# Optimization experiments

Hardware: AMD Instinct MI355X
Metric: run time of the kernel (lower is better)

## Reference

```python
import jax, jax.numpy as jnp
import numpy as np

N_NODES = 20000
NEG_SLOPE = 0.2
EPS = 1e-10


def _gat_reparam_layer(x, W, att_i, att_j, bias, src, dst, heads, c2):
    """GATConv (PyG-style, aggr='add') whose output encodes (mean, std) per head,
    followed by diag-Gaussian reparameterization with N(0,1) prior (eval mode:
    output = mean; ixz = KL(q||p) summed over channels, averaged over heads).
    x: [N, F]; W: [F, heads*c2]; att_i/att_j: [heads, c2]; bias: [heads*c2].
    c2 = 2 * out_channels (mean + std logits).
    Returns out [N, heads*(c2//2)], ixz [N]."""
    N = x.shape[0]
    h = (x @ W).reshape(N, heads, c2)                      # [N, H, 2C]
    h_i = h[dst]                                           # [E, H, 2C] target (x_i)
    h_j = h[src]                                           # [E, H, 2C] source (x_j)
    # attention logits: leaky_relu((x_i*att_i).sum + (x_j*att_j).sum)
    logits = jnp.sum(h_i * att_i, axis=-1) + jnp.sum(h_j * att_j, axis=-1)  # [E, H]
    logits = jax.nn.leaky_relu(logits, NEG_SLOPE)
    # segment softmax over incoming edges of each target node
    lmax = jax.ops.segment_max(logits, dst, num_segments=N)  # [N, H]
    ex = jnp.exp(logits - lmax[dst])                         # [E, H]
    denom = jax.ops.segment_sum(ex, dst, num_segments=N)     # [N, H]
    alpha = ex / denom[dst]                                  # [E, H]
    # weighted scatter-add aggregation
    msg = alpha[:, :, None] * h_j                            # [E, H, 2C]
    out = jax.ops.segment_sum(msg, dst, num_segments=N)      # [N, H, 2C]
    out = out + bias.reshape(1, heads, c2)
    # reparameterization: split per head into mean / std
    C = c2 // 2
    mean = out[..., :C]                                      # [N, H, C]
    std = jax.nn.softplus(out[..., C:]) + EPS                # [N, H, C]
    # KL(N(mean, std) || N(0, 1)) per element, sum over C, mean over heads
    kl = 0.5 * (std * std + mean * mean - 1.0) - jnp.log(std)
    ixz = kl.sum(-1).mean(-1)                                # [N]
    return mean.reshape(N, heads * C), ixz


def setup_inputs() -> dict:
    key = jax.random.key(0)
    ks = jax.random.split(key, 10)
    N, F1 = N_NODES, 256
    E = 320000
    H1, C1 = 8, 32    # conv1: latent_size//2 = 32 per head, doubled for (mean,std)
    H2, C2 = 1, 16    # conv2: num_classes = 16
    edge_index = jax.random.randint(ks[0], (2, E), 0, N, dtype=jnp.int32)
    s = 0.1
    return {
        "x": jax.random.normal(ks[1], (N, F1), jnp.float32),
        "edge_index": edge_index,
        "W1": jax.random.normal(ks[2], (F1, H1 * 2 * C1), jnp.float32) * s,
        "att_i1": jax.random.normal(ks[3], (H1, 2 * C1), jnp.float32) * s,
        "att_j1": jax.random.normal(ks[4], (H1, 2 * C1), jnp.float32) * s,
        "bias1": jax.random.normal(ks[5], (H1 * 2 * C1,), jnp.float32) * s,
        "W2": jax.random.normal(ks[6], (H1 * C1, H2 * 2 * C2), jnp.float32) * s,
        "att_i2": jax.random.normal(ks[7], (H2, 2 * C2), jnp.float32) * s,
        "att_j2": jax.random.normal(ks[8], (H2, 2 * C2), jnp.float32) * s,
        "bias2": jax.random.normal(ks[9], (H2 * 2 * C2,), jnp.float32) * s,
    }


def reference(x, edge_index, W1, att_i1, att_j1, bias1, W2, att_i2, att_j2, bias2):
    src, dst = edge_index[0], edge_index[1]
    # eval mode: dropout is identity, output = posterior mean (val_use_mean=True)
    h1, ixz1 = _gat_reparam_layer(x, W1, att_i1, att_j1, bias1, src, dst, heads=8, c2=64)
    h1 = jax.nn.elu(h1)
    h2, ixz2 = _gat_reparam_layer(h1, W2, att_i2, att_j2, bias2, src, dst, heads=1, c2=32)
    return h2
```

## Files before the change

kernel.cpp:

```cpp
#include <hip/hip_runtime.h>
#include <hip/hip_bf16.h>

#define NN 20000
#define EE 320000
#define NEG_SLOPE 0.2f
#define CAP1 96
#define BCAP 128

typedef unsigned short u16;
typedef short bf16x8 __attribute__((ext_vector_type(8)));
typedef unsigned short u16x8 __attribute__((ext_vector_type(8)));
typedef float f32x4 __attribute__((ext_vector_type(4)));

__device__ __forceinline__ u16 f2bf(float f) {
    unsigned u = __float_as_uint(f);
    return (u16)((u + 0x7FFFu + ((u >> 16) & 1u)) >> 16);
}
__device__ __forceinline__ float bf2f(u16 b) { return __uint_as_float(((unsigned)b) << 16); }

__device__ __forceinline__ void lds_fence() {
    asm volatile("s_waitcnt lgkmcnt(0)" ::: "memory");
}

__device__ __forceinline__ void gld_lds16(const u16* g, u16* l) {
    __builtin_amdgcn_global_load_lds(
        (__attribute__((address_space(1))) void*)g,
        (__attribute__((address_space(3))) void*)l, 16, 0, 0);
}

#define IB_W1 320
#define IB_W2 338
#define IB_CU 417
#define IB_XB 2917
__global__ __launch_bounds__(256) void init_pack(
    const float* __restrict__ x,
    const float* __restrict__ W1, const float* __restrict__ atti1, const float* __restrict__ attj1,
    const float* __restrict__ W2, const float* __restrict__ atti2, const float* __restrict__ attj2,
    u16* __restrict__ Wp1, u16* __restrict__ Wp2, int* __restrict__ cursor, u16* __restrict__ xb)
{
    int b = blockIdx.x;
    if (b < IB_W1) {
        int t = b*256 + threadIdx.x;
        int k = t & 255, j = t >> 8;
        float v = 0.f;
        if (j < 256) {
            v = W1[(size_t)k*512 + ((j>>5)*64 + (j&31))];
        } else if (j < 264) {
            int h = j - 256; float s = 0.f;
            for (int c = 0; c < 64; ++c) s += W1[(size_t)k*512 + h*64 + c] * atti1[h*64 + c];
            v = s;
        } else if (j < 272) {
            int h = j - 264; float s = 0.f;
            for (int c = 0; c < 64; ++c) s += W1[(size_t)k*512 + h*64 + c] * attj1[h*64 + c];
            v = s;
        }
        Wp1[t] = f2bf(v);
    } else if (b < IB_W2) {
        int j = b - IB_W1;
        int k = threadIdx.x;
        float v;
        if (j < 16) {
            v = W2[(size_t)k*32 + j];
        } else if (j == 16) {
            float s = 0.f; for (int c = 0; c < 32; ++c) s += W2[(size_t)k*32 + c] * atti2[c]; v = s;
        } else {
            float s = 0.f; for (int c = 0; c < 32; ++c) s += W2[(size_t)k*32 + c] * attj2[c]; v = s;
        }
        Wp2[j*256 + k] = f2bf(v);
    } else if (b < IB_CU) {
        int i = (b - IB_W2)*256 + threadIdx.x;
        if (i < NN) cursor[i] = 0;
    } else {
        size_t gb = ((size_t)(b - IB_CU)*256 + threadIdx.x) * 8;
        float4 v0 = *(const float4*)&x[gb];
        float4 v1 = *(const float4*)&x[gb + 4];
        u16x8 u;
        u[0]=f2bf(v0.x); u[1]=f2bf(v0.y); u[2]=f2bf(v0.z); u[3]=f2bf(v0.w);
        u[4]=f2bf(v1.x); u[5]=f2bf(v1.y); u[6]=f2bf(v1.z); u[7]=f2bf(v1.w);
        *(u16x8*)&xb[gb] = u;
    }
}

__device__ __forceinline__ void gemm_body(
    int bx, int by, int tid,
    const u16* __restrict__ Ab, const u16* __restrict__ Bp, int M,
    u16* __restrict__ outB, float* __restrict__ outAi, float* __restrict__ outAj)
{
    __shared__ __align__(16) u16 lsA[64*64];
    __shared__ __align__(16) u16 lsB[64*64];

    const int w    = tid >> 6, lane = tid & 63;
    const int brow = by * 64, bcol = bx * 64;

    const int r0 = 2*w*8     + (lane >> 3);
    const int r1 = (2*w+1)*8 + (lane >> 3);
    const int sl = lane & 7;
    const size_t aOff0 = (size_t)min(brow + r0, M-1)*256 + ((sl ^ (r0 & 7))*8);
    const size_t aOff1 = (size_t)min(brow + r1, M-1)*256 + ((sl ^ (r1 & 7))*8);
    const size_t bOff0 = (size_t)(bcol + r0)*256 + ((sl ^ (r0 & 7))*8);
    const size_t bOff1 = (size_t)(bcol + r1)*256 + ((sl ^ (r1 & 7))*8);
    u16* ldsA0 = lsA + (2*w)*512;
    u16* ldsA1 = lsA + (2*w+1)*512;
    u16* ldsB0 = lsB + (2*w)*512;
    u16* ldsB1 = lsB + (2*w+1)*512;

    const int frow = (w << 4) + (lane & 15);
    const int fkb  = lane >> 4;
    int aF[2], bF[2][4];
    #pragma unroll
    for (int v = 0; v < 2; ++v) {
        aF[v] = frow*64 + (((v*4 + fkb) ^ (frow & 7)))*8;
        #pragma unroll
        for (int tt = 0; tt < 4; ++tt) {
            int col = tt*16 + (lane & 15);
            bF[v][tt] = col*64 + (((v*4 + fkb) ^ (col & 7)))*8;
        }
    }

    f32x4 acc[4] = {};

    for (int ks = 0; ks < 4; ++ks) {
        const int k0 = ks*64;
        gld_lds16(Ab + aOff0 + k0, ldsA0);
        gld_lds16(Ab + aOff1 + k0, ldsA1);
        gld_lds16(Bp + bOff0 + k0, ldsB0);
        gld_lds16(Bp + bOff1 + k0, ldsB1);
        __syncthreads();
        #pragma unroll
        for (int v = 0; v < 2; ++v) {
            bf16x8 a = *(const bf16x8*)&lsA[aF[v]];
            #pragma unroll
            for (int tt = 0; tt < 4; ++tt) {
                bf16x8 b = *(const bf16x8*)&lsB[bF[v][tt]];
                acc[tt] = __builtin_amdgcn_mfma_f32_16x16x32_bf16(a, b, acc[tt], 0, 0, 0);
            }
        }
        __syncthreads();
    }

    #pragma unroll
    for (int tt = 0; tt < 4; ++tt) {
        int col = bcol + tt*16 + (lane & 15);
        #pragma unroll
        for (int r = 0; r < 4; ++r) {
            int row = brow + (w << 4) + ((lane >> 4) << 2) + r;
            if (row >= M) continue;
            float v = acc[tt][r];
            if      (col < 256) outB[(size_t)row*256 + col] = f2bf(v);
            else if (col < 264) outAi[(size_t)row*8 + (col - 256)] = v;
            else if (col < 272) outAj[(size_t)row*8 + (col - 264)] = v;
        }
    }
}

#define G1_BLOCKS 1565
#define SC_BLOCKS 1250

__global__ __launch_bounds__(256) void fusedA(
    const u16* __restrict__ xb, const u16* __restrict__ Wp1,
    u16* __restrict__ h1m, float* __restrict__ ai1, float* __restrict__ aj1,
    const int* __restrict__ src, const int* __restrict__ dst,
    int* __restrict__ cursor, int* __restrict__ elist)
{
    int b = blockIdx.x;
    if (b < G1_BLOCKS) {
        gemm_body(b % 5, b / 5, threadIdx.x, xb, Wp1, NN, h1m, ai1, aj1);
    } else {
        int e = (b - G1_BLOCKS)*256 + threadIdx.x;
        if (e < EE) {
            int d = dst[e];
            int pos = atomicAdd(&cursor[d], 1);
            if (pos < BCAP) elist[d*BCAP + pos] = src[e];
        }
    }
}

__global__ __launch_bounds__(256) void gat1g2(
    const int* __restrict__ cursor, const int* __restrict__ elist,
    const float* __restrict__ ai, const float* __restrict__ aj,
    const u16* __restrict__ h1m, const float* __restrict__ bias,
    const u16* __restrict__ Wp2,
    float* __restrict__ h2m, float* __restrict__ ai2, float* __restrict__ aj2)
{
    __shared__ float s_w[4][CAP1*9];
    __shared__ int   s_src[4][CAP1];
    __shared__ float s_inv[4][8];

    const int wv = threadIdx.x >> 6, lane = threadIdx.x & 63;
    const int n = blockIdx.x*4 + wv;
    const int beg = n*BCAP;
    const int deg = min(cursor[n], BCAP);
    float* sw = s_w[wv];
    int*   ss = s_src[wv];

    const int g = lane & 31, head = g >> 2, cbase = (g & 3)*8;
    float v[8];

    if (deg <= CAP1) {
        {
            int hq = lane & 3, eo = lane >> 2;
            float2 aip = *(const float2*)&ai[(size_t)n*8 + hq*2];
            float sm0 = 0.f, sm1 = 0.f;
            for (int e = eo; e < deg; e += 16) {
                int s = elist[beg + e];
                if (hq == 0) ss[e] = s;
                float2 a = *(const float2*)&aj[(size_t)s*8 + hq*2];
                float l0 = aip.x + a.x;
                float l1 = aip.y + a.y;
                l0 = (l0 >= 0.f) ? l0 : NEG_SLOPE * l0;
                l1 = (l1 >= 0.f) ? l1 : NEG_SLOPE * l1;
                float ex0 = __expf(l0), ex1 = __expf(l1);
                sw[e*9 + 2*hq]     = ex0;
                sw[e*9 + 2*hq + 1] = ex1;
                sm0 += ex0; sm1 += ex1;
            }
            #pragma unroll
            for (int o = 4; o <= 32; o <<= 1) {
                sm0 += __shfl_xor(sm0, o, 64);
                sm1 += __shfl_xor(sm1, o, 64);
            }
            if (eo == 0) {
                s_inv[wv][2*hq]     = (deg > 0) ? 1.f / sm0 : 0.f;
                s_inv[wv][2*hq + 1] = (deg > 0) ? 1.f / sm1 : 0.f;
            }
        }
        lds_fence();
        {
            int slot = lane >> 5;
            float inv = s_inv[wv][head];
            const u16* hb = h1m + (size_t)g*8;
            float acc[8] = {};
            int e = slot;
            for (; e + 6 < deg; e += 8) {
                int   i0 = ss[e],          i1 = ss[e+2],          i2 = ss[e+4],          i3 = ss[e+6];
                float w0 = sw[e*9+head],   w1 = sw[(e+2)*9+head], w2 = sw[(e+4)*9+head], w3 = sw[(e+6)*9+head];
                bf16x8 v0 = *(const bf16x8*)&hb[(size_t)i0*256];
                bf16x8 v1 = *(const bf16x8*)&hb[(size_t)i1*256];
                bf16x8 v2 = *(const bf16x8*)&hb[(size_t)i2*256];
                bf16x8 v3 = *(const bf16x8*)&hb[(size_t)i3*256];
                #pragma unroll
                for (int k = 0; k < 8; ++k) {
                    acc[k] += w0 * bf2f((u16)v0[k]);
                    acc[k] += w1 * bf2f((u16)v1[k]);
                    acc[k] += w2 * bf2f((u16)v2[k]);
                    acc[k] += w3 * bf2f((u16)v3[k]);
                }
            }
            for (; e < deg; e += 2) {
                float wgt = sw[e*9 + head];
                bf16x8 vx = *(const bf16x8*)&hb[(size_t)ss[e]*256];
                #pragma unroll
                for (int k = 0; k < 8; ++k)
                    acc[k] += wgt * bf2f((u16)vx[k]);
            }
            #pragma unroll
            for (int k = 0; k < 8; ++k) acc[k] += __shfl_xor(acc[k], 32, 64);
            #pragma unroll
            for (int k = 0; k < 8; ++k) {
                float t = acc[k]*inv + bias[head*64 + cbase + k];
                v[k] = (t > 0.f) ? t : (__expf(t) - 1.0f);
            }
        }
    } else {
        float* sh = sw;
        float4 ai0 = *(const float4*)&ai[(size_t)n*8];
        float4 ai1v = *(const float4*)&ai[(size_t)n*8 + 4];
        float aiv[8] = {ai0.x,ai0.y,ai0.z,ai0.w,ai1v.x,ai1v.y,ai1v.z,ai1v.w};
        for (int h = 0; h < 8; ++h) {
            float a_i = aiv[h];
            float mx = -INFINITY;
            for (int e = lane; e < deg; e += 64) {
                int s = elist[beg + e];
                float t = a_i + aj[(size_t)s*8 + h];
                t = (t >= 0.f) ? t : NEG_SLOPE * t;
                mx = fmaxf(mx, t);
            }
            #pragma unroll
            for (int o = 32; o > 0; o >>= 1) mx = fmaxf(mx, __shfl_xor(mx, o, 64));
            float sm = 0.f;
            for (int e = lane; e < deg; e += 64) {
                int s = elist[beg + e];
                float t = a_i + aj[(size_t)s*8 + h];
                t = (t >= 0.f) ? t : NEG_SLOPE * t;
                sm += __expf(t - mx);
            }
            #pragma unroll
            for (int o = 32; o > 0; o >>= 1) sm += __shfl_xor(sm, o, 64);
            float inv = (deg > 0) ? 1.f / sm : 0.f;
            int c = lane & 31, sl2 = lane >> 5;
            float a2 = 0.f;
            for (int e = sl2; e < deg; e += 2) {
                int s = elist[beg + e];
                float t = a_i + aj[(size_t)s*8 + h];
                t = (t >= 0.f) ? t : NEG_SLOPE * t;
                float wgt = __expf(t - mx);
                a2 += wgt * bf2f(h1m[(size_t)s*256 + h*32 + c]);
            }
            a2 += __shfl_xor(a2, 32, 64);
            if (lane < 32) {
                float t = a2*inv + bias[h*64 + c];
                sh[h*32 + c] = (t > 0.f) ? t : (__expf(t) - 1.0f);
            }
        }
        lds_fence();
        #pragma unroll
        for (int k = 0; k < 8; ++k) v[k] = sh[g*8 + k];
    }

    {
        int jbase = (lane >> 5) * 9;
        float p[9];
        #pragma unroll
        for (int jj = 0; jj < 9; ++jj) {
            u16x8 wr = *(const u16x8*)&Wp2[(size_t)(jbase + jj)*256 + g*8];
            float s = 0.f;
            #pragma unroll
            for (int k = 0; k < 8; ++k) s += v[k] * bf2f((u16)wr[k]);
            p[jj] = s;
        }
        #pragma unroll
        for (int o = 1; o < 32; o <<= 1) {
            #pragma unroll
            for (int jj = 0; jj < 9; ++jj) p[jj] += __shfl_xor(p[jj], o, 64);
        }
        float outv = p[0];
        #pragma unroll
        for (int jj = 1; jj < 9; ++jj) if (g == jj) outv = p[jj];
        if (g < 9) {
            int j = jbase + g;
            if      (j < 16)  h2m[(size_t)n*16 + j] = outv;
            else if (j == 16) ai2[n] = outv;
            else if (j == 17) aj2[n] = outv;
        }
    }
}

__global__ __launch_bounds__(256) void gat2_fused(
    const int* __restrict__ cursor, const int* __restrict__ elist,
    const float* __restrict__ ai, const float* __restrict__ aj,
    const float* __restrict__ h2m, const float* __restrict__ bias,
    float* __restrict__ outp)
{
    __shared__ float s_w2[4][64];
    __shared__ int   s_s2[4][64];

    const int wv = threadIdx.x >> 6, lane = threadIdx.x & 63;
    const int n = blockIdx.x*4 + wv;
    const int beg = n*BCAP;
    const int deg = min(cursor[n], BCAP);
    float a_i = ai[n];

    if (deg <= 64) {
        float ex = 0.f; int s = 0;
        if (lane < deg) {
            s = elist[beg + lane];
            float t = a_i + aj[s];
            t = (t >= 0.f) ? t : NEG_SLOPE * t;
            ex = __expf(t);
        }
        float sm = ex;
        #pragma unroll
        for (int o = 32; o > 0; o >>= 1) sm += __shfl_xor(sm, o, 64);
        float inv = (deg > 0) ? 1.f / sm : 0.f;
        if (lane < deg) { s_w2[wv][lane] = ex; s_s2[wv][lane] = s; }
        lds_fence();
        int c4 = lane & 3, slot = lane >> 2;
        float4 acc = make_float4(0.f, 0.f, 0.f, 0.f);
        for (int e = slot; e < deg; e += 16) {
            float w = s_w2[wv][e];
            int sv = s_s2[wv][e];
            float4 vv = *(const float4*)&h2m[(size_t)sv*16 + c4*4];
            acc.x += w*vv.x; acc.y += w*vv.y; acc.z += w*vv.z; acc.w += w*vv.w;
        }
        #pragma unroll
        for (int o = 4; o <= 32; o <<= 1) {
            acc.x += __shfl_xor(acc.x, o, 64);
            acc.y += __shfl_xor(acc.y, o, 64);
            acc.z += __shfl_xor(acc.z, o, 64);
            acc.w += __shfl_xor(acc.w, o, 64);
        }
        if (lane < 4) {
            const float4 b4 = *(const float4*)&bias[lane*4];
            float4 r = make_float4(acc.x*inv + b4.x, acc.y*inv + b4.y,
                                   acc.z*inv + b4.z, acc.w*inv + b4.w);
            *(float4*)&outp[(size_t)n*16 + lane*4] = r;
        }
    } else {
        float mx = -INFINITY;
        for (int e = lane; e < deg; e += 64) {
            int s2 = elist[beg + e];
            float t = a_i + aj[s2];
            t = (t >= 0.f) ? t : NEG_SLOPE * t;
            mx = fmaxf(mx, t);
        }
        #pragma unroll
        for (int o = 32; o > 0; o >>= 1) mx = fmaxf(mx, __shfl_xor(mx, o, 64));
        float sm = 0.f;
        for (int e = lane; e < deg; e += 64) {
            int s2 = elist[beg + e];
            float t = a_i + aj[s2];
            t = (t >= 0.f) ? t : NEG_SLOPE * t;
            sm += __expf(t - mx);
        }
        #pragma unroll
        for (int o = 32; o > 0; o >>= 1) sm += __shfl_xor(sm, o, 64);
        float inv = (deg > 0) ? 1.f / sm : 0.f;
        int c = lane & 15, e4 = lane >> 4;
        float acc = 0.f;
        for (int e = e4; e < deg; e += 4) {
            int s2 = elist[beg + e];
            float t = a_i + aj[s2];
            t = (t >= 0.f) ? t : NEG_SLOPE * t;
            float w = __expf(t - mx);
            acc += w * h2m[(size_t)s2*16 + c];
        }
        acc += __shfl_xor(acc, 16, 64);
        acc += __shfl_xor(acc, 32, 64);
        if (lane < 16) outp[(size_t)n*16 + lane] = acc*inv + bias[lane];
    }
}

static inline size_t al16(size_t x) { return (x + 15) & ~(size_t)15; }

extern "C" void kernel_launch(void* const* d_in, const int* in_sizes, int n_in,
                              void* d_out, int out_size, void* d_ws, size_t ws_size,
                              hipStream_t stream) {
    const float* x      = (const float*)d_in[0];
    const int*   ei     = (const int*)  d_in[1];
    const float* W1     = (const float*)d_in[2];
    const float* att_i1 = (const float*)d_in[3];
    const float* att_j1 = (const float*)d_in[4];
    const float* bias1  = (const float*)d_in[5];
    const float* W2     = (const float*)d_in[6];
    const float* att_i2 = (const float*)d_in[7];
    const float* att_j2 = (const float*)d_in[8];
    const float* bias2  = (const float*)d_in[9];
    float* out = (float*)d_out;

    const int N = NN, E = EE;
    const int* src = ei;
    const int* dst = ei + E;

    char* p = (char*)d_ws;
    #define CARVE(ty, name, elems) ty* name = (ty*)p; p += al16((size_t)(elems) * sizeof(ty));
    CARVE(u16,   Wp1,  320*256)
    CARVE(u16,   Wp2,  18*256)
    CARVE(u16,   xb,   (size_t)N*256)
    CARVE(u16,   h1m,  (size_t)N*256)
    CARVE(float, ai1,  (size_t)N*8)
    CARVE(float, aj1,  (size_t)N*8)
    CARVE(float, h2m,  (size_t)N*16)
    CARVE(float, ai2,  N)
    CARVE(float, aj2,  N)
    CARVE(int,   cursor,   N)
    CARVE(int,   elist,    (size_t)N*BCAP)
    #undef CARVE

    const int BS = 256;

    init_pack<<<IB_XB, BS, 0, stream>>>(x, W1, att_i1, att_j1, W2, att_i2, att_j2,
                                        Wp1, Wp2, cursor, xb);

    fusedA<<<G1_BLOCKS + SC_BLOCKS, BS, 0, stream>>>(xb, Wp1, h1m, ai1, aj1,
                                                     src, dst, cursor, elist);

    gat1g2<<<N/4, BS, 0, stream>>>(cursor, elist, ai1, aj1, h1m, bias1, Wp2,
                                   h2m, ai2, aj2);

    gat2_fused<<<N/4, BS, 0, stream>>>(cursor, elist, ai2, aj2, h2m, bias2, out);
}
```

Measured before the change: 77.52 us.

## Prefetch neighbor feature gathers before softmax weights in GAT aggregation kernels

Both aggregation kernels now load each edge's source index once per lane and broadcast it with shuffles. The first 16 (layer 1) or all 64 (layer 2) neighbor feature rows are gathered into registers before the attention exponentials and sums are computed, so the gather latency overlaps the softmax work. Layer 1 now computes all 8 heads' logits per lane with a full-wave shuffle reduction in place of the quad-strided LDS layout. CAP1 drops from 96 to 64, which sends nodes with degree 65-96 to the slower general path, and the register prefetch raises VGPR pressure.

```diff
diff --git a/kernel.cpp b/kernel.cpp
--- a/kernel.cpp
+++ b/kernel.cpp
@@ -4,7 +4,7 @@
 #define NN 20000
 #define EE 320000
 #define NEG_SLOPE 0.2f
-#define CAP1 96
+#define CAP1 64
 #define BCAP 128
 
 typedef unsigned short u16;
@@ -184,7 +184,6 @@
 {
     __shared__ float s_w[4][CAP1*9];
     __shared__ int   s_src[4][CAP1];
-    __shared__ float s_inv[4][8];
 
     const int wv = threadIdx.x >> 6, lane = threadIdx.x & 63;
     const int n = blockIdx.x*4 + wv;
@@ -194,72 +193,99 @@
     int*   ss = s_src[wv];
 
     const int g = lane & 31, head = g >> 2, cbase = (g & 3)*8;
+    const int slot = lane >> 5;
     float v[8];
 
     if (deg <= CAP1) {
+        const bool has = lane < deg;
+        int s_own = 0;
+        if (has) s_own = elist[beg + lane];
+        if (has) ss[lane] = s_own;
+
+        float4 a0 = make_float4(0.f,0.f,0.f,0.f), a1 = a0;
+        if (has) {
+            a0 = *(const float4*)&aj[(size_t)s_own*8];
+            a1 = *(const float4*)&aj[(size_t)s_own*8 + 4];
+        }
+
+        const u16* hb = h1m + (size_t)g*8;
+        bf16x8 vv[8];
+        #pragma unroll
+        for (int j = 0; j < 8; ++j) {
+            int ej = slot + 2*j;
+            int sj = __shfl(s_own, ej);
+            if (ej < deg) vv[j] = *(const bf16x8*)&hb[(size_t)sj*256];
+        }
+
+        float4 ai0 = *(const float4*)&ai[(size_t)n*8];
+        float4 ai1v = *(const float4*)&ai[(size_t)n*8 + 4];
+        float ex[8];
         {
-            int hq = lane & 3, eo = lane >> 2;
-            float2 aip = *(const float2*)&ai[(size_t)n*8 + hq*2];
-            float sm0 = 0.f, sm1 = 0.f;
-            for (int e = eo; e < deg; e += 16) {
-                int s = elist[beg + e];
-                if (hq == 0) ss[e] = s;
-                float2 a = *(const float2*)&aj[(size_t)s*8 + hq*2];
-                float l0 = aip.x + a.x;
-                float l1 = aip.y + a.y;
-                l0 = (l0 >= 0.f) ? l0 : NEG_SLOPE * l0;
-                l1 = (l1 >= 0.f) ? l1 : NEG_SLOPE * l1;
-                float ex0 = __expf(l0), ex1 = __expf(l1);
-                sw[e*9 + 2*hq]     = ex0;
-                sw[e*9 + 2*hq + 1] = ex1;
-                sm0 += ex0; sm1 += ex1;
-            }
-            #pragma unroll
-            for (int o = 4; o <= 32; o <<= 1) {
-                sm0 += __shfl_xor(sm0, o, 64);
-                sm1 += __shfl_xor(sm1, o, 64);
-            }
-            if (eo == 0) {
-                s_inv[wv][2*hq]     = (deg > 0) ? 1.f / sm0 : 0.f;
-                s_inv[wv][2*hq + 1] = (deg > 0) ? 1.f / sm1 : 0.f;
-            }
-        }
+            float av[8] = {a0.x,a0.y,a0.z,a0.w,a1.x,a1.y,a1.z,a1.w};
+            float aiv[8] = {ai0.x,ai0.y,ai0.z,ai0.w,ai1v.x,ai1v.y,ai1v.z,ai1v.w};
+            #pragma unroll
+            for (int h = 0; h < 8; ++h) {
+                float l = aiv[h] + av[h];
+                l = (l >= 0.f) ? l : NEG_SLOPE * l;
+                ex[h] = has ? __expf(l) : 0.f;
+                sw[lane*9 + h] = ex[h];
+            }
+        }
+        #pragma unroll
+        for (int o = 1; o <= 32; o <<= 1) {
+            #pragma unroll
+            for (int h = 0; h < 8; ++h) ex[h] += __shfl_xor(ex[h], o, 64);
+        }
+        float smh = ex[0];
+        if (head == 1) smh = ex[1];
+        if (head == 2) smh = ex[2];
+        if (head == 3) smh = ex[3];
+        if (head == 4) smh = ex[4];
+        if (head == 5) smh = ex[5];
+        if (head == 6) smh = ex[6];
+        if (head == 7) smh = ex[7];
+        float inv = (deg > 0) ? 1.f / smh : 0.f;
+
         lds_fence();
-        {
-            int slot = lane >> 5;
-            float inv = s_inv[wv][head];
-            const u16* hb = h1m + (size_t)g*8;
-            float acc[8] = {};
-            int e = slot;
-            for (; e + 6 < deg; e += 8) {
-                int   i0 = ss[e],          i1 = ss[e+2],          i2 = ss[e+4],          i3 = ss[e+6];
-                float w0 = sw[e*9+head],   w1 = sw[(e+2)*9+head], w2 = sw[(e+4)*9+head], w3 = sw[(e+6)*9+head];
-                bf16x8 v0 = *(const bf16x8*)&hb[(size_t)i0*256];
-                bf16x8 v1 = *(const bf16x8*)&hb[(size_t)i1*256];
-                bf16x8 v2 = *(const bf16x8*)&hb[(size_t)i2*256];
-                bf16x8 v3 = *(const bf16x8*)&hb[(size_t)i3*256];
+
+        float acc[8] = {};
+        #pragma unroll
+        for (int j = 0; j < 8; ++j) {
+            int ej = slot + 2*j;
+            if (ej < deg) {
+                float w = sw[ej*9 + head];
                 #pragma unroll
-                for (int k = 0; k < 8; ++k) {
-                    acc[k] += w0 * bf2f((u16)v0[k]);
-                    acc[k] += w1 * bf2f((u16)v1[k]);
-                    acc[k] += w2 * bf2f((u16)v2[k]);
-                    acc[k] += w3 * bf2f((u16)v3[k]);
-                }
-            }
-            for (; e < deg; e += 2) {
-                float wgt = sw[e*9 + head];
-                bf16x8 vx = *(const bf16x8*)&hb[(size_t)ss[e]*256];
-                #pragma unroll
-                for (int k = 0; k < 8; ++k)
-                    acc[k] += wgt * bf2f((u16)vx[k]);
-            }
-            #pragma unroll
-            for (int k = 0; k < 8; ++k) acc[k] += __shfl_xor(acc[k], 32, 64);
+                for (int k = 0; k < 8; ++k) acc[k] += w * bf2f((u16)vv[j][k]);
+            }
+        }
+        int e = 16 + slot;
+        for (; e + 6 < deg; e += 8) {
+            int   i0 = ss[e],          i1 = ss[e+2],          i2 = ss[e+4],          i3 = ss[e+6];
+            float w0 = sw[e*9+head],   w1 = sw[(e+2)*9+head], w2 = sw[(e+4)*9+head], w3 = sw[(e+6)*9+head];
+            bf16x8 v0 = *(const bf16x8*)&hb[(size_t)i0*256];
+            bf16x8 v1 = *(const bf16x8*)&hb[(size_t)i1*256];
+            bf16x8 v2 = *(const bf16x8*)&hb[(size_t)i2*256];
+            bf16x8 v3 = *(const bf16x8*)&hb[(size_t)i3*256];
             #pragma unroll
             for (int k = 0; k < 8; ++k) {
-                float t = acc[k]*inv + bias[head*64 + cbase + k];
-                v[k] = (t > 0.f) ? t : (__expf(t) - 1.0f);
-            }
+                acc[k] += w0 * bf2f((u16)v0[k]);
+                acc[k] += w1 * bf2f((u16)v1[k]);
+                acc[k] += w2 * bf2f((u16)v2[k]);
+                acc[k] += w3 * bf2f((u16)v3[k]);
+            }
+        }
+        for (; e < deg; e += 2) {
+            float wgt = sw[e*9 + head];
+            bf16x8 vx = *(const bf16x8*)&hb[(size_t)ss[e]*256];
+            #pragma unroll
+            for (int k = 0; k < 8; ++k) acc[k] += wgt * bf2f((u16)vx[k]);
+        }
+        #pragma unroll
+        for (int k = 0; k < 8; ++k) acc[k] += __shfl_xor(acc[k], 32, 64);
+        #pragma unroll
+        for (int k = 0; k < 8; ++k) {
+            float t = acc[k]*inv + bias[head*64 + cbase + k];
+            v[k] = (t > 0.f) ? t : (__expf(t) - 1.0f);
         }
     } else {
         float* sh = sw;
@@ -342,7 +368,6 @@
     float* __restrict__ outp)
 {
     __shared__ float s_w2[4][64];
-    __shared__ int   s_s2[4][64];
 
     const int wv = threadIdx.x >> 6, lane = threadIdx.x & 63;
     const int n = blockIdx.x*4 + wv;
@@ -351,26 +376,40 @@
     float a_i = ai[n];
 
     if (deg <= 64) {
-        float ex = 0.f; int s = 0;
-        if (lane < deg) {
-            s = elist[beg + lane];
-            float t = a_i + aj[s];
+        const bool has = lane < deg;
+        int s_own = 0;
+        if (has) s_own = elist[beg + lane];
+
+        const int c4 = lane & 3, slot = lane >> 2;
+        float4 vv[4];
+        #pragma unroll
+        for (int j = 0; j < 4; ++j) {
+            int ej = slot + 16*j;
+            int sj = __shfl(s_own, ej);
+            if (ej < deg) vv[j] = *(const float4*)&h2m[(size_t)sj*16 + c4*4];
+        }
+
+        float ex = 0.f;
+        if (has) {
+            float t = a_i + aj[s_own];
             t = (t >= 0.f) ? t : NEG_SLOPE * t;
             ex = __expf(t);
         }
+        s_w2[wv][lane] = ex;
         float sm = ex;
         #pragma unroll
         for (int o = 32; o > 0; o >>= 1) sm += __shfl_xor(sm, o, 64);
         float inv = (deg > 0) ? 1.f / sm : 0.f;
-        if (lane < deg) { s_w2[wv][lane] = ex; s_s2[wv][lane] = s; }
         lds_fence();
-        int c4 = lane & 3, slot = lane >> 2;
+
         float4 acc = make_float4(0.f, 0.f, 0.f, 0.f);
-        for (int e = slot; e < deg; e += 16) {
-            float w = s_w2[wv][e];
-            int sv = s_s2[wv][e];
-            float4 vv = *(const float4*)&h2m[(size_t)sv*16 + c4*4];
-            acc.x += w*vv.x; acc.y += w*vv.y; acc.z += w*vv.z; acc.w += w*vv.w;
+        #pragma unroll
+        for (int j = 0; j < 4; ++j) {
+            int ej = slot + 16*j;
+            if (ej < deg) {
+                float w = s_w2[wv][ej];
+                acc.x += w*vv[j].x; acc.y += w*vv[j].y; acc.z += w*vv[j].z; acc.w += w*vv[j].w;
+            }
         }
         #pragma unroll
         for (int o = 4; o <= 32; o <<= 1) {
```

After: 95.01 us. +22.6%, slower.
